# Optimization experiments

Hardware: AMD Instinct MI355X
Metric: run time of the kernel (lower is better)

## Reference

```python
import jax, jax.numpy as jnp
import numpy as np

N = 50000   # nodes
E = 800000  # edges
H = 128     # hidden_dim
H2 = H // 2


def setup_inputs() -> dict:
    key = jax.random.key(0)
    ks = jax.random.split(key, 12)
    s = 0.05  # weight scale for numerical sanity
    d = {}
    d['coord_x'] = jax.random.normal(ks[0], (N,), jnp.float32)
    d['coord_y'] = jax.random.normal(ks[1], (N,), jnp.float32)
    d['W1'] = jax.random.normal(ks[2], (3, H), jnp.float32) * s
    d['b1'] = jnp.zeros((H,), jnp.float32)
    d['W2'] = jax.random.normal(ks[3], (H, H), jnp.float32) * s
    d['b2'] = jnp.zeros((H,), jnp.float32)
    d['W3'] = jax.random.normal(ks[4], (H, H), jnp.float32) * s
    d['b3'] = jnp.zeros((H,), jnp.float32)
    d['W4'] = jax.random.normal(ks[5], (H, H), jnp.float32) * s
    d['b4'] = jnp.zeros((H,), jnp.float32)
    d['W5'] = jax.random.normal(ks[6], (H, H), jnp.float32) * s
    d['b5'] = jnp.zeros((H,), jnp.float32)
    d['Wl1'] = jax.random.normal(ks[7], (H, H2), jnp.float32) * s
    d['bl1'] = jnp.zeros((H2,), jnp.float32)
    d['Wl2'] = jax.random.normal(ks[8], (H2, 1), jnp.float32) * s
    d['bl2'] = jnp.zeros((1,), jnp.float32)
    d['src'] = jax.random.randint(ks[9], (E,), 0, N, dtype=jnp.int32)
    d['dst'] = jax.random.randint(ks[10], (E,), 0, N, dtype=jnp.int32)
    return d


def reference(coord_x, coord_y, W1, b1, W2, b2, W3, b3, W4, b4, W5, b5,
              Wl1, bl1, Wl2, bl2, src, dst):
    ones_e = jnp.ones((E,), jnp.float32)
    in_deg = jax.ops.segment_sum(ones_e, dst, num_segments=N)   # [N]
    out_deg = jax.ops.segment_sum(ones_e, src, num_segments=N)  # [N]
    # DGL GraphConv norm='both': D_out^{-1/2} on src side, D_in^{-1/2} on dst side,
    # degrees clamped to min 1.
    norm_s = (jnp.maximum(out_deg, 1.0) ** -0.5)[:, None]  # [N,1]
    norm_d = (jnp.maximum(in_deg, 1.0) ** -0.5)[:, None]   # [N,1]

    def gconv(h, W, b):
        msg = (h * norm_s)[src]                                   # [E,F] gather
        agg = jax.ops.segment_sum(msg, dst, num_segments=N)       # [N,F] scatter-add
        return (agg * norm_d) @ W + b

    # node features: [in_degree, x, y]
    h = jnp.stack([in_deg, coord_x, coord_y], axis=1)  # [N,3]
    for W, b in ((W1, b1), (W2, b2), (W3, b3), (W4, b4), (W5, b5)):
        h = jax.nn.relu(gconv(h, W, b))

    graph_emb = jnp.mean(h, axis=0, keepdims=True)          # [1,H] mean_nodes
    h_emb = jax.nn.relu(graph_emb @ Wl1 + bl1)              # dropout p=0 -> identity
    pred = jax.nn.sigmoid(h_emb @ Wl2 + bl2)                # [1,1]
    return pred, graph_emb, h
```

## Files before the change

kernel.cpp:

```cpp
#include <hip/hip_runtime.h>
#include <hip/hip_bf16.h>
#include <math.h>

#define NN 50000
#define NE 800000
#define HD 128
#define NB 196
#define CAP 5120
#define B1_EPB 1024

typedef __attribute__((ext_vector_type(8))) short bf16x8v;
typedef __attribute__((ext_vector_type(4))) float f32x4v;

static __device__ __forceinline__ unsigned short f2bf(float x) {
    union { float f; unsigned u; } v; v.f = x;
    unsigned r = v.u + 0x7fff + ((v.u >> 16) & 1);
    return (unsigned short)(r >> 16);
}

__global__ __launch_bounds__(256) void bucket_kernel(const int* __restrict__ src,
                                                     const int* __restrict__ dst,
                                                     int* __restrict__ dcur,
                                                     int* __restrict__ scur,
                                                     int2* __restrict__ dbucket,
                                                     int* __restrict__ sbucket) {
    __shared__ int hd[NB], hsb[NB], cd[NB], cs[NB];
    int t = threadIdx.x;
    if (t < NB) { hd[t] = 0; hsb[t] = 0; }
    __syncthreads();
    int d[4], s[4];
    int e0 = blockIdx.x * B1_EPB + t;
    #pragma unroll
    for (int j = 0; j < 4; ++j) {
        int e = e0 + j * 256;
        if (e < NE) {
            d[j] = dst[e]; s[j] = src[e];
            atomicAdd(&hd[d[j] >> 8], 1);
            atomicAdd(&hsb[s[j] >> 8], 1);
        } else d[j] = -1;
    }
    __syncthreads();
    if (t < NB) {
        cd[t] = atomicAdd(&dcur[t], hd[t]);
        cs[t] = atomicAdd(&scur[t], hsb[t]);
    }
    __syncthreads();
    #pragma unroll
    for (int j = 0; j < 4; ++j) {
        if (d[j] >= 0) {
            int b = d[j] >> 8;
            int p = atomicAdd(&cd[b], 1);
            if (p < CAP) dbucket[(long)b * CAP + p] = make_int2(d[j], s[j]);
            int bs = s[j] >> 8;
            int p2 = atomicAdd(&cs[bs], 1);
            if (p2 < CAP) sbucket[(long)bs * CAP + p2] = s[j];
        }
    }
}

__global__ __launch_bounds__(256) void csr_out_kernel(const int2* __restrict__ dbucket,
                                                      const int* __restrict__ dcur,
                                                      const int* __restrict__ sbucket,
                                                      const int* __restrict__ scur,
                                                      int* __restrict__ row_ptr,
                                                      int* __restrict__ col,
                                                      int* __restrict__ out_cnt) {
    __shared__ int buf[256];
    __shared__ int hist[256];
    __shared__ int cur[256];
    int k = blockIdx.x, t = threadIdx.x;

    int tot = (t < NB) ? min(dcur[t], CAP) : 0;
    buf[t] = tot;
    __syncthreads();
    for (int o = 1; o < 256; o <<= 1) {
        int a = (t >= o) ? buf[t - o] : 0;
        __syncthreads();
        buf[t] += a;
        __syncthreads();
    }
    int base = (k > 0) ? buf[k - 1] : 0;
    int cnt = min(dcur[k], CAP);

    hist[t] = 0;
    __syncthreads();
    const int2* bk = dbucket + (long)k * CAP;
    for (int e = t; e < cnt; e += 256) atomicAdd(&hist[bk[e].x & 255], 1);
    __syncthreads();
    int h = hist[t];

    buf[t] = h;
    __syncthreads();
    for (int o = 1; o < 256; o <<= 1) {
        int a = (t >= o) ? buf[t - o] : 0;
        __syncthreads();
        buf[t] += a;
        __syncthreads();
    }
    int start = base + buf[t] - h;
    int id = (k << 8) + t;
    if (id < NN) row_ptr[id] = start;
    if (k == NB - 1 && t == 0) row_ptr[NN] = base + cnt;
    cur[t] = start;
    __syncthreads();

    for (int e = t; e < cnt; e += 256) {
        int2 p = bk[e];
        int pos = atomicAdd(&cur[p.x & 255], 1);
        col[pos] = p.y;
    }

    __syncthreads();
    hist[t] = 0;
    __syncthreads();
    int scnt = min(scur[k], CAP);
    const int* sk = sbucket + (long)k * CAP;
    for (int e = t; e < scnt; e += 256) atomicAdd(&hist[sk[e] & 255], 1);
    __syncthreads();
    if (id < NN) out_cnt[id] = hist[t];
}

__global__ __launch_bounds__(256) void initw_kernel(const float* __restrict__ cx,
                                                    const float* __restrict__ cy,
                                                    const int* __restrict__ row_ptr,
                                                    const int* __restrict__ out_cnt,
                                                    const float* __restrict__ W2,
                                                    const float* __restrict__ W3,
                                                    const float* __restrict__ W4,
                                                    const float* __restrict__ W5,
                                                    float* __restrict__ norm_s,
                                                    float* __restrict__ norm_d,
                                                    float* __restrict__ h0s,
                                                    unsigned short* __restrict__ Wt,
                                                    float* __restrict__ embsum) {
    int bid = blockIdx.x, t = threadIdx.x;
    if (bid < NB) {
        int i = (bid << 8) + t;
        if (i < NN) {
            float id = (float)(row_ptr[i + 1] - row_ptr[i]);
            float od = (float)out_cnt[i];
            float ns = 1.0f / sqrtf(fmaxf(od, 1.0f));
            norm_s[i] = ns;
            norm_d[i] = 1.0f / sqrtf(fmaxf(id, 1.0f));
            h0s[i * 3 + 0] = id * ns;
            h0s[i * 3 + 1] = cx[i] * ns;
            h0s[i * 3 + 2] = cy[i] * ns;
        }
    } else {
        int gid = ((bid - NB) << 8) + t;
        int l = gid >> 14, idx = gid & 16383;
        int n = idx >> 7, k = idx & 127;
        const float* W = (l == 0) ? W2 : (l == 1) ? W3 : (l == 2) ? W4 : W5;
        Wt[gid] = f2bf(W[k * 128 + n]);
        if (bid == NB && t < 128) embsum[t] = 0.0f;
    }
}

__global__ __launch_bounds__(256) void gather3_kernel(const int* __restrict__ row_ptr,
                                                      const int* __restrict__ col,
                                                      const float* __restrict__ h0s,
                                                      const float* __restrict__ norm_d,
                                                      float* __restrict__ agg3) {
    int n = blockIdx.x * 256 + threadIdx.x;
    if (n < NN) {
        float a0 = 0.f, a1 = 0.f, a2 = 0.f;
        int end = row_ptr[n + 1];
        for (int e = row_ptr[n]; e < end; ++e) {
            int s = col[e];
            a0 += h0s[s * 3 + 0];
            a1 += h0s[s * 3 + 1];
            a2 += h0s[s * 3 + 2];
        }
        float nd = norm_d[n];
        agg3[n * 3 + 0] = a0 * nd;
        agg3[n * 3 + 1] = a1 * nd;
        agg3[n * 3 + 2] = a2 * nd;
    }
}

__global__ __launch_bounds__(256) void node3_kernel(const float* __restrict__ agg3,
                                                    const float* __restrict__ norm_s,
                                                    const float* __restrict__ W1,
                                                    const float* __restrict__ b1,
                                                    unsigned short* __restrict__ h1s) {
    int gid = blockIdx.x * 256 + threadIdx.x;
    int i = gid >> 7, c = gid & 127;
    if (i < NN) {
        float a0 = agg3[i * 3 + 0];
        float a1 = agg3[i * 3 + 1];
        float a2 = agg3[i * 3 + 2];
        float v = a0 * W1[c] + a1 * W1[128 + c] + a2 * W1[256 + c] + b1[c];
        h1s[i * 128 + c] = f2bf(fmaxf(v, 0.0f) * norm_s[i]);
    }
}

__global__ __launch_bounds__(256) void gather_bf16_kernel(const int* __restrict__ row_ptr,
                                                          const int* __restrict__ col,
                                                          const unsigned int* __restrict__ hs2,
                                                          const float* __restrict__ norm_d,
                                                          unsigned int* __restrict__ aggb2) {
    int t = threadIdx.x;
    int wave = t >> 6;
    int lane = t & 63;
    int n = blockIdx.x * 4 + wave;
    if (n >= NN) return;
    int beg = row_ptr[n], end = row_ptr[n + 1];
    float nd = norm_d[n];
    const unsigned int* hb = hs2 + lane;
    float ax = 0.f, ay = 0.f;
    int e = beg;
    for (; e + 7 < end; e += 8) {
        unsigned u[8];
        #pragma unroll
        for (int j = 0; j < 8; ++j) u[j] = hb[(long)col[e + j] << 6];
        #pragma unroll
        for (int j = 0; j < 8; ++j) {
            ax += __uint_as_float(u[j] << 16);
            ay += __uint_as_float(u[j] & 0xffff0000u);
        }
    }
    for (; e < end; ++e) {
        unsigned u0 = hb[(long)col[e] << 6];
        ax += __uint_as_float(u0 << 16);
        ay += __uint_as_float(u0 & 0xffff0000u);
    }
    unsigned po = (unsigned)f2bf(ax * nd) | ((unsigned)f2bf(ay * nd) << 16);
    aggb2[(n << 6) + lane] = po;
}

__global__ __launch_bounds__(256) void gemm_mfma_kernel(const unsigned short* __restrict__ aggb,
                                                        const float* __restrict__ scale,
                                                        const unsigned short* __restrict__ Wt,
                                                        const float* __restrict__ bias,
                                                        unsigned short* __restrict__ out_bf,
                                                        float* __restrict__ out_f32,
                                                        float* __restrict__ embsum) {
    __shared__ unsigned short ldsw[128][136];
    __shared__ float ldscol[4][4][128];

    int t = threadIdx.x;
    int wv = t >> 6, lane = t & 63;
    int fr = lane & 15, kq = lane >> 4;
    int m0 = blockIdx.x * 64 + wv * 16;

    #pragma unroll
    for (int i = 0; i < 8; ++i) {
        int idx = t + 256 * i;
        int r = idx >> 4;
        int c8 = (idx & 15) << 3;
        *(bf16x8v*)(&ldsw[r][c8]) = *(const bf16x8v*)(Wt + (r << 7) + c8);
    }

    int mrow = m0 + fr;
    long abase = (long)((mrow < NN) ? mrow : 0) << 7;
    bf16x8v a0 = *(const bf16x8v*)(aggb + abase + 0  + kq * 8);
    bf16x8v a1 = *(const bf16x8v*)(aggb + abase + 32 + kq * 8);
    bf16x8v a2 = *(const bf16x8v*)(aggb + abase + 64 + kq * 8);
    bf16x8v a3 = *(const bf16x8v*)(aggb + abase + 96 + kq * 8);

    float sc[4];
    #pragma unroll
    for (int r = 0; r < 4; ++r) {
        int mr = m0 + kq * 4 + r;
        sc[r] = (out_bf && mr < NN) ? scale[mr] : 1.0f;
    }

    __syncthreads();

    #pragma unroll
    for (int nt = 0; nt < 8; ++nt) {
        int n0 = nt << 4;
        f32x4v acc = {0.f, 0.f, 0.f, 0.f};
        acc = __builtin_amdgcn_mfma_f32_16x16x32_bf16(a0, *(const bf16x8v*)(&ldsw[n0 + fr][0  + kq * 8]), acc, 0, 0, 0);
        acc = __builtin_amdgcn_mfma_f32_16x16x32_bf16(a1, *(const bf16x8v*)(&ldsw[n0 + fr][32 + kq * 8]), acc, 0, 0, 0);
        acc = __builtin_amdgcn_mfma_f32_16x16x32_bf16(a2, *(const bf16x8v*)(&ldsw[n0 + fr][64 + kq * 8]), acc, 0, 0, 0);
        acc = __builtin_amdgcn_mfma_f32_16x16x32_bf16(a3, *(const bf16x8v*)(&ldsw[n0 + fr][96 + kq * 8]), acc, 0, 0, 0);

        int c = n0 + fr;
        float bv = bias[c];
        float cs = 0.f;
        #pragma unroll
        for (int r = 0; r < 4; ++r) {
            int mr = m0 + kq * 4 + r;
            if (mr < NN) {
                float v = fmaxf(acc[r] + bv, 0.f);
                if (out_bf) out_bf[((long)mr << 7) + c] = f2bf(v * sc[r]);
                else        out_f32[((long)mr << 7) + c] = v;
                cs += v;
            }
        }
        if (embsum) ldscol[wv][kq][c] = cs;
    }

    if (embsum) {
        __syncthreads();
        if (t < 128) {
            float s = 0.f;
            #pragma unroll
            for (int w = 0; w < 4; ++w)
                #pragma unroll
                for (int q = 0; q < 4; ++q)
                    s += ldscol[w][q][t];
            atomicAdd(&embsum[t], s);
        }
    }
}

__global__ __launch_bounds__(128) void head_kernel(const float* __restrict__ embsum,
                                                   const float* __restrict__ Wl1,
                                                   const float* __restrict__ bl1,
                                                   const float* __restrict__ Wl2,
                                                   const float* __restrict__ bl2,
                                                   float* __restrict__ d_out) {
    __shared__ float emb[128];
    __shared__ float hemb[64];
    int t = threadIdx.x;
    float e = embsum[t] * (1.0f / (float)NN);
    emb[t] = e;
    d_out[1 + t] = e;
    __syncthreads();
    if (t < 64) {
        float acc = bl1[t];
        for (int k = 0; k < 128; ++k)
            acc += emb[k] * Wl1[k * 64 + t];
        hemb[t] = fmaxf(acc, 0.f);
    }
    __syncthreads();
    if (t == 0) {
        float acc = bl2[0];
        for (int j = 0; j < 64; ++j)
            acc += hemb[j] * Wl2[j];
        d_out[0] = 1.0f / (1.0f + expf(-acc));
    }
}

extern "C" void kernel_launch(void* const* d_in, const int* in_sizes, int n_in,
                              void* d_out, int out_size, void* d_ws, size_t ws_size,
                              hipStream_t stream) {
    const float* cx  = (const float*)d_in[0];
    const float* cy  = (const float*)d_in[1];
    const float* W1  = (const float*)d_in[2];
    const float* b1  = (const float*)d_in[3];
    const float* W2  = (const float*)d_in[4];
    const float* b2  = (const float*)d_in[5];
    const float* W3  = (const float*)d_in[6];
    const float* b3  = (const float*)d_in[7];
    const float* W4  = (const float*)d_in[8];
    const float* b4  = (const float*)d_in[9];
    const float* W5  = (const float*)d_in[10];
    const float* b5  = (const float*)d_in[11];
    const float* Wl1 = (const float*)d_in[12];
    const float* bl1 = (const float*)d_in[13];
    const float* Wl2 = (const float*)d_in[14];
    const float* bl2 = (const float*)d_in[15];
    const int*   src = (const int*)d_in[16];
    const int*   dst = (const int*)d_in[17];

    float* out = (float*)d_out;
    float* h_out = out + 129;

    float* ws       = (float*)d_ws;
    float* norm_s   = ws;
    float* norm_d   = ws + NN;
    int*   out_cnt  = (int*)(ws + 2 * NN);
    int*   row_ptr  = (int*)(ws + 3 * NN);
    unsigned short* hs   = (unsigned short*)(ws + 4 * NN + 64);
    unsigned short* aggb = (unsigned short*)(ws + 68 * NN + 64);
    int*   col      = (int*)(ws + 132 * NN + 64);
    float* h0s      = ws + 148 * NN + 64;
    float* agg3     = ws + 151 * NN + 64;
    unsigned short* Wt = (unsigned short*)(ws + 154 * NN + 64);
    float* embsum   = ws + 154 * NN + 64 + 32768;
    int*   dcur     = (int*)(ws + 154 * NN + 33600);
    int*   scur     = dcur + NB;
    int2*  dbucket  = (int2*)(ws + 154 * NN + 34048);
    int*   sbucket  = (int*)(ws + 154 * NN + 34048 + 2 * NB * CAP);

    hipMemsetAsync(dcur, 0, 2 * NB * sizeof(int), stream);
    bucket_kernel<<<(NE + B1_EPB - 1) / B1_EPB, 256, 0, stream>>>(src, dst, dcur, scur,
                                                                  dbucket, sbucket);
    csr_out_kernel<<<NB, 256, 0, stream>>>(dbucket, dcur, sbucket, scur,
                                           row_ptr, col, out_cnt);

    initw_kernel<<<NB + 256, 256, 0, stream>>>(cx, cy, row_ptr, out_cnt,
                                               W2, W3, W4, W5,
                                               norm_s, norm_d, h0s, Wt, embsum);

    gather3_kernel<<<(NN + 255) / 256, 256, 0, stream>>>(row_ptr, col, h0s, norm_d, agg3);
    node3_kernel<<<(NN * 128) / 256, 256, 0, stream>>>(agg3, norm_s, W1, b1, hs);

    const float* bs[4] = {b2, b3, b4, b5};
    const int gather_blocks = (NN + 3) / 4;
    const int gemm_blocks = (NN + 63) / 64;
    for (int l = 0; l < 4; ++l) {
        gather_bf16_kernel<<<gather_blocks, 256, 0, stream>>>(row_ptr, col,
                                                              (const unsigned int*)hs,
                                                              norm_d,
                                                              (unsigned int*)aggb);
        bool last = (l == 3);
        gemm_mfma_kernel<<<gemm_blocks, 256, 0, stream>>>(
            aggb, norm_s, Wt + l * 16384, bs[l],
            last ? nullptr : hs,
            last ? h_out : nullptr,
            last ? embsum : nullptr);
    }

    head_kernel<<<1, 128, 0, stream>>>(embsum, Wl1, bl1, Wl2, bl2, out);
}
```

Baseline: 330.3 us.

## Fuse gather and MFMA GEMM per layer, shrink edge indices to 16-bit

For hidden layers 2-4, the separate gather and GEMM kernels become one kernel. It aggregates 16 nodes into LDS and runs bf16 MFMA directly, so the intermediate aggregate buffer no longer makes a global round trip. Node indices in buckets and in the CSR column array are stored as unsigned shorts, which halves index traffic. Node IDs up to 50000 fit in 16 bits, but this caps the node count at 65535. The fused kernel reads the weights from global memory in every block, and each block covers only 16 rows, which may reduce weight reuse.

```diff
diff --git a/kernel.cpp b/kernel.cpp
--- a/kernel.cpp
+++ b/kernel.cpp
@@ -22,8 +22,8 @@
                                                      const int* __restrict__ dst,
                                                      int* __restrict__ dcur,
                                                      int* __restrict__ scur,
-                                                     int2* __restrict__ dbucket,
-                                                     int* __restrict__ sbucket) {
+                                                     ushort2* __restrict__ dbucket,
+                                                     unsigned short* __restrict__ sbucket) {
     __shared__ int hd[NB], hsb[NB], cd[NB], cs[NB];
     int t = threadIdx.x;
     if (t < NB) { hd[t] = 0; hsb[t] = 0; }
@@ -50,20 +50,21 @@
         if (d[j] >= 0) {
             int b = d[j] >> 8;
             int p = atomicAdd(&cd[b], 1);
-            if (p < CAP) dbucket[(long)b * CAP + p] = make_int2(d[j], s[j]);
+            if (p < CAP) dbucket[(long)b * CAP + p] = make_ushort2((unsigned short)d[j],
+                                                                   (unsigned short)s[j]);
             int bs = s[j] >> 8;
             int p2 = atomicAdd(&cs[bs], 1);
-            if (p2 < CAP) sbucket[(long)bs * CAP + p2] = s[j];
-        }
-    }
-}
-
-__global__ __launch_bounds__(256) void csr_out_kernel(const int2* __restrict__ dbucket,
+            if (p2 < CAP) sbucket[(long)bs * CAP + p2] = (unsigned short)s[j];
+        }
+    }
+}
+
+__global__ __launch_bounds__(256) void csr_out_kernel(const ushort2* __restrict__ dbucket,
                                                       const int* __restrict__ dcur,
-                                                      const int* __restrict__ sbucket,
+                                                      const unsigned short* __restrict__ sbucket,
                                                       const int* __restrict__ scur,
                                                       int* __restrict__ row_ptr,
-                                                      int* __restrict__ col,
+                                                      unsigned short* __restrict__ col,
                                                       int* __restrict__ out_cnt) {
     __shared__ int buf[256];
     __shared__ int hist[256];
@@ -84,7 +85,7 @@
 
     hist[t] = 0;
     __syncthreads();
-    const int2* bk = dbucket + (long)k * CAP;
+    const ushort2* bk = dbucket + (long)k * CAP;
     for (int e = t; e < cnt; e += 256) atomicAdd(&hist[bk[e].x & 255], 1);
     __syncthreads();
     int h = hist[t];
@@ -105,7 +106,7 @@
     __syncthreads();
 
     for (int e = t; e < cnt; e += 256) {
-        int2 p = bk[e];
+        ushort2 p = bk[e];
         int pos = atomicAdd(&cur[p.x & 255], 1);
         col[pos] = p.y;
     }
@@ -114,7 +115,7 @@
     hist[t] = 0;
     __syncthreads();
     int scnt = min(scur[k], CAP);
-    const int* sk = sbucket + (long)k * CAP;
+    const unsigned short* sk = sbucket + (long)k * CAP;
     for (int e = t; e < scnt; e += 256) atomicAdd(&hist[sk[e] & 255], 1);
     __syncthreads();
     if (id < NN) out_cnt[id] = hist[t];
@@ -157,7 +158,7 @@
 }
 
 __global__ __launch_bounds__(256) void gather3_kernel(const int* __restrict__ row_ptr,
-                                                      const int* __restrict__ col,
+                                                      const unsigned short* __restrict__ col,
                                                       const float* __restrict__ h0s,
                                                       const float* __restrict__ norm_d,
                                                       float* __restrict__ agg3) {
@@ -194,8 +195,79 @@
     }
 }
 
+__global__ __launch_bounds__(256) void fused_layer16_kernel(const int* __restrict__ row_ptr,
+                                                            const unsigned short* __restrict__ col,
+                                                            const unsigned int* __restrict__ hin,
+                                                            const float* __restrict__ norm_d,
+                                                            const float* __restrict__ norm_s,
+                                                            const unsigned short* __restrict__ Wt,
+                                                            const float* __restrict__ bias,
+                                                            unsigned short* __restrict__ hout) {
+    __shared__ unsigned int lA[16][68];
+    int t = threadIdx.x;
+    int wv = t >> 6, lane = t & 63;
+    int m0 = blockIdx.x << 4;
+
+    const unsigned int* hb = hin + lane;
+    #pragma unroll
+    for (int i = 0; i < 4; ++i) {
+        int r = (i << 2) + wv;
+        int n = m0 + r;
+        int beg = row_ptr[n], end = row_ptr[n + 1];
+        float nd = norm_d[n];
+        float ax = 0.f, ay = 0.f;
+        int e = beg;
+        for (; e + 7 < end; e += 8) {
+            unsigned u[8];
+            #pragma unroll
+            for (int j = 0; j < 8; ++j) u[j] = hb[(long)col[e + j] << 6];
+            #pragma unroll
+            for (int j = 0; j < 8; ++j) {
+                ax += __uint_as_float(u[j] << 16);
+                ay += __uint_as_float(u[j] & 0xffff0000u);
+            }
+        }
+        for (; e < end; ++e) {
+            unsigned u0 = hb[(long)col[e] << 6];
+            ax += __uint_as_float(u0 << 16);
+            ay += __uint_as_float(u0 & 0xffff0000u);
+        }
+        lA[r][lane] = (unsigned)f2bf(ax * nd) | ((unsigned)f2bf(ay * nd) << 16);
+    }
+    __syncthreads();
+
+    int fr = lane & 15, kq = lane >> 4;
+    bf16x8v a0 = *(const bf16x8v*)&lA[fr][ 0 + (kq << 2)];
+    bf16x8v a1 = *(const bf16x8v*)&lA[fr][16 + (kq << 2)];
+    bf16x8v a2 = *(const bf16x8v*)&lA[fr][32 + (kq << 2)];
+    bf16x8v a3 = *(const bf16x8v*)&lA[fr][48 + (kq << 2)];
+
+    float4 scv = *(const float4*)(norm_s + m0 + (kq << 2));
+
+    #pragma unroll
+    for (int j = 0; j < 2; ++j) {
+        int n0 = ((wv << 1) + j) << 4;
+        const unsigned short* wb = Wt + ((n0 + fr) << 7) + (kq << 3);
+        f32x4v acc = {0.f, 0.f, 0.f, 0.f};
+        acc = __builtin_amdgcn_mfma_f32_16x16x32_bf16(a0, *(const bf16x8v*)(wb + 0),  acc, 0, 0, 0);
+        acc = __builtin_amdgcn_mfma_f32_16x16x32_bf16(a1, *(const bf16x8v*)(wb + 32), acc, 0, 0, 0);
+        acc = __builtin_amdgcn_mfma_f32_16x16x32_bf16(a2, *(const bf16x8v*)(wb + 64), acc, 0, 0, 0);
+        acc = __builtin_amdgcn_mfma_f32_16x16x32_bf16(a3, *(const bf16x8v*)(wb + 96), acc, 0, 0, 0);
+
+        int c = n0 + fr;
+        float bv = bias[c];
+        #pragma unroll
+        for (int r = 0; r < 4; ++r) {
+            int mr = m0 + (kq << 2) + r;
+            float v = fmaxf(acc[r] + bv, 0.f);
+            float sc = (r == 0) ? scv.x : (r == 1) ? scv.y : (r == 2) ? scv.z : scv.w;
+            hout[((long)mr << 7) + c] = f2bf(v * sc);
+        }
+    }
+}
+
 __global__ __launch_bounds__(256) void gather_bf16_kernel(const int* __restrict__ row_ptr,
-                                                          const int* __restrict__ col,
+                                                          const unsigned short* __restrict__ col,
                                                           const unsigned int* __restrict__ hs2,
                                                           const float* __restrict__ norm_d,
                                                           unsigned int* __restrict__ aggb2) {
@@ -229,10 +301,8 @@
 }
 
 __global__ __launch_bounds__(256) void gemm_mfma_kernel(const unsigned short* __restrict__ aggb,
-                                                        const float* __restrict__ scale,
                                                         const unsigned short* __restrict__ Wt,
                                                         const float* __restrict__ bias,
-                                                        unsigned short* __restrict__ out_bf,
                                                         float* __restrict__ out_f32,
                                                         float* __restrict__ embsum) {
     __shared__ unsigned short ldsw[128][136];
@@ -257,13 +327,6 @@
     bf16x8v a1 = *(const bf16x8v*)(aggb + abase + 32 + kq * 8);
     bf16x8v a2 = *(const bf16x8v*)(aggb + abase + 64 + kq * 8);
     bf16x8v a3 = *(const bf16x8v*)(aggb + abase + 96 + kq * 8);
-
-    float sc[4];
-    #pragma unroll
-    for (int r = 0; r < 4; ++r) {
-        int mr = m0 + kq * 4 + r;
-        sc[r] = (out_bf && mr < NN) ? scale[mr] : 1.0f;
-    }
 
     __syncthreads();
 
@@ -284,25 +347,22 @@
             int mr = m0 + kq * 4 + r;
             if (mr < NN) {
                 float v = fmaxf(acc[r] + bv, 0.f);
-                if (out_bf) out_bf[((long)mr << 7) + c] = f2bf(v * sc[r]);
-                else        out_f32[((long)mr << 7) + c] = v;
+                out_f32[((long)mr << 7) + c] = v;
                 cs += v;
             }
         }
-        if (embsum) ldscol[wv][kq][c] = cs;
-    }
-
-    if (embsum) {
-        __syncthreads();
-        if (t < 128) {
-            float s = 0.f;
+        ldscol[wv][kq][c] = cs;
+    }
+
+    __syncthreads();
+    if (t < 128) {
+        float s = 0.f;
+        #pragma unroll
+        for (int w = 0; w < 4; ++w)
             #pragma unroll
-            for (int w = 0; w < 4; ++w)
-                #pragma unroll
-                for (int q = 0; q < 4; ++q)
-                    s += ldscol[w][q][t];
-            atomicAdd(&embsum[t], s);
-        }
+            for (int q = 0; q < 4; ++q)
+                s += ldscol[w][q][t];
+        atomicAdd(&embsum[t], s);
     }
 }
 
@@ -364,17 +424,17 @@
     float* norm_d   = ws + NN;
     int*   out_cnt  = (int*)(ws + 2 * NN);
     int*   row_ptr  = (int*)(ws + 3 * NN);
-    unsigned short* hs   = (unsigned short*)(ws + 4 * NN + 64);
-    unsigned short* aggb = (unsigned short*)(ws + 68 * NN + 64);
-    int*   col      = (int*)(ws + 132 * NN + 64);
+    unsigned short* hsA = (unsigned short*)(ws + 4 * NN + 64);
+    unsigned short* hsB = (unsigned short*)(ws + 68 * NN + 64);
+    unsigned short* col = (unsigned short*)(ws + 132 * NN + 64);
     float* h0s      = ws + 148 * NN + 64;
     float* agg3     = ws + 151 * NN + 64;
     unsigned short* Wt = (unsigned short*)(ws + 154 * NN + 64);
     float* embsum   = ws + 154 * NN + 64 + 32768;
     int*   dcur     = (int*)(ws + 154 * NN + 33600);
     int*   scur     = dcur + NB;
-    int2*  dbucket  = (int2*)(ws + 154 * NN + 34048);
-    int*   sbucket  = (int*)(ws + 154 * NN + 34048 + 2 * NB * CAP);
+    ushort2* dbucket = (ushort2*)(ws + 154 * NN + 34048);
+    unsigned short* sbucket = (unsigned short*)(ws + 154 * NN + 34048 + NB * CAP);
 
     hipMemsetAsync(dcur, 0, 2 * NB * sizeof(int), stream);
     bucket_kernel<<<(NE + B1_EPB - 1) / B1_EPB, 256, 0, stream>>>(src, dst, dcur, scur,
@@ -387,23 +447,25 @@
                                                norm_s, norm_d, h0s, Wt, embsum);
 
     gather3_kernel<<<(NN + 255) / 256, 256, 0, stream>>>(row_ptr, col, h0s, norm_d, agg3);
-    node3_kernel<<<(NN * 128) / 256, 256, 0, stream>>>(agg3, norm_s, W1, b1, hs);
-
-    const float* bs[4] = {b2, b3, b4, b5};
-    const int gather_blocks = (NN + 3) / 4;
-    const int gemm_blocks = (NN + 63) / 64;
-    for (int l = 0; l < 4; ++l) {
-        gather_bf16_kernel<<<gather_blocks, 256, 0, stream>>>(row_ptr, col,
-                                                              (const unsigned int*)hs,
-                                                              norm_d,
-                                                              (unsigned int*)aggb);
-        bool last = (l == 3);
-        gemm_mfma_kernel<<<gemm_blocks, 256, 0, stream>>>(
-            aggb, norm_s, Wt + l * 16384, bs[l],
-            last ? nullptr : hs,
-            last ? h_out : nullptr,
-            last ? embsum : nullptr);
-    }
+    node3_kernel<<<(NN * 128) / 256, 256, 0, stream>>>(agg3, norm_s, W1, b1, hsA);
+
+    const float* bs[3] = {b2, b3, b4};
+    unsigned short* hcur = hsA;
+    unsigned short* hnxt = hsB;
+    for (int l = 0; l < 3; ++l) {
+        fused_layer16_kernel<<<NN / 16, 256, 0, stream>>>(row_ptr, col,
+                                                          (const unsigned int*)hcur,
+                                                          norm_d, norm_s,
+                                                          Wt + l * 16384, bs[l], hnxt);
+        unsigned short* tmp = hcur; hcur = hnxt; hnxt = tmp;
+    }
+
+    gather_bf16_kernel<<<(NN + 3) / 4, 256, 0, stream>>>(row_ptr, col,
+                                                         (const unsigned int*)hcur,
+                                                         norm_d,
+                                                         (unsigned int*)hnxt);
+    gemm_mfma_kernel<<<(NN + 63) / 64, 256, 0, stream>>>(hnxt, Wt + 3 * 16384, b5,
+                                                         h_out, embsum);
 
     head_kernel<<<1, 128, 0, stream>>>(embsum, Wl1, bl1, Wl2, bl2, out);
 }
```

New measurement: 316.4 us. 4.2% less time.
